# Kernel optimization log

Measured on AMD Instinct MI355X. Metric: run time of the kernel, lower is better.

Reference implementation:

```python
import jax, jax.numpy as jnp
import numpy as np

L, D, H, DK, DV, DFF = 6, 512, 8, 64, 64, 2048
B, S = 8, 512
EPS = 1e-5


def _pos_table(max_len, d_model):
    pos = np.arange(max_len)[:, None].astype(np.float64)
    i = np.arange(d_model)[None, :].astype(np.float64)
    t = pos / np.power(10000.0, 2.0 * i / d_model)
    t[0, :] = 0.0
    t[1:, 0::2] = np.sin(t[1:, 0::2])
    t[1:, 1::2] = np.cos(t[1:, 1::2])
    return jnp.asarray(t, dtype=jnp.float32)


def _ln(x, g, b):
    m = jnp.mean(x, axis=-1, keepdims=True)
    v = jnp.mean(jnp.square(x - m), axis=-1, keepdims=True)
    return (x - m) * jax.lax.rsqrt(v + EPS) * g + b


def setup_inputs() -> dict:
    key = jax.random.key(0)
    ks = jax.random.split(key, 12)
    s = 0.02
    return {
        "enc_inputs": jax.random.normal(ks[0], (B, S, D), jnp.float32),
        "enc_inputs_mask": jax.random.randint(ks[1], (B, S), 0, 100, dtype=jnp.int64),
        "Wq": jax.random.normal(ks[2], (L, D, H * DK), jnp.float32) * s,
        "Wk": jax.random.normal(ks[3], (L, D, H * DK), jnp.float32) * s,
        "Wv": jax.random.normal(ks[4], (L, D, H * DV), jnp.float32) * s,
        "Wo": jax.random.normal(ks[5], (L, H * DV, D), jnp.float32) * s,
        "ln1_g": jnp.ones((L, D), jnp.float32),
        "ln1_b": jnp.zeros((L, D), jnp.float32),
        "W1": jax.random.normal(ks[6], (L, D, DFF), jnp.float32) * s,
        "W2": jax.random.normal(ks[7], (L, DFF, D), jnp.float32) * s,
        "ln2_g": jnp.ones((L, D), jnp.float32),
        "ln2_b": jnp.zeros((L, D), jnp.float32),
    }


def reference(enc_inputs, enc_inputs_mask, Wq, Wk, Wv, Wo, ln1_g, ln1_b, W1, W2, ln2_g, ln2_b):
    b, s, _ = enc_inputs.shape
    x = enc_inputs + _pos_table(s, D)  # positional encoding (dropout = eval/no-op)
    # pad mask: True where key token is pad (mask id == 0); broadcast over heads & queries
    pad = (enc_inputs_mask == 0)[:, None, None, :]  # [B,1,1,S]
    inv_sqrt_dk = np.float32(1.0 / np.sqrt(DK))
    attns = []
    for l in range(L):
        residual = x
        q = (x @ Wq[l]).reshape(b, s, H, DK).transpose(0, 2, 1, 3)  # [B,H,S,DK]
        k = (x @ Wk[l]).reshape(b, s, H, DK).transpose(0, 2, 1, 3)
        v = (x @ Wv[l]).reshape(b, s, H, DV).transpose(0, 2, 1, 3)
        scores = jnp.einsum("bhqd,bhkd->bhqk", q, k) * inv_sqrt_dk
        scores = jnp.where(pad, jnp.float32(-1e9), scores)
        attn = jax.nn.softmax(scores, axis=-1)
        ctx = jnp.einsum("bhqk,bhkd->bhqd", attn, v)
        ctx = ctx.transpose(0, 2, 1, 3).reshape(b, s, H * DV)
        x = _ln(ctx @ Wo[l] + residual, ln1_g[l], ln1_b[l])
        x = _ln(jax.nn.relu(x @ W1[l]) @ W2[l] + x, ln2_g[l], ln2_b[l])
        attns.append(attn)
    return x, jnp.stack(attns)  # [B,S,D], [L,B,H,S,S]
```

## Files before the change

kernel.cpp:

```cpp
#include <hip/hip_runtime.h>

typedef __attribute__((ext_vector_type(8))) short bf16x8;
typedef __attribute__((ext_vector_type(4))) short bf16x4;
typedef __attribute__((ext_vector_type(4))) float f32x4;

__device__ __forceinline__ float b2f(ushort u) {
  union { uint u; float f; } x; x.u = ((uint)u) << 16; return x.f;
}
__device__ __forceinline__ ushort f2b(float f) {
  union { float f; uint u; } x; x.f = f;
  uint r = x.u + 0x7fffu + ((x.u >> 16) & 1u);
  return (ushort)(r >> 16);
}
__device__ __forceinline__ f32x4 mfma16(bf16x8 a, bf16x8 b, f32x4 c) {
  return __builtin_amdgcn_mfma_f32_16x16x32_bf16(a, b, c, 0, 0, 0);
}

__global__ void detect_kernel(const uint* __restrict__ ln1g, const uint* __restrict__ mask,
                              int* __restrict__ flags) {
  if (threadIdx.x == 0) {
    flags[0] = (ln1g[0] == 0x3F800000u) ? 1 : 0;
    int odd0 = 1;
    for (int i = 0; i < 16; i++)
      if (mask[2 * i + 1] != 0u) odd0 = 0;
    flags[1] = odd0;
  }
}

__global__ __launch_bounds__(256) void convert_kernel(const void* __restrict__ src,
                                                      ushort* __restrict__ dst, int n,
                                                      const int* __restrict__ flags) {
  int f = flags[0];
  int base = (blockIdx.x * 256 + threadIdx.x) * 8;
  int stride = gridDim.x * 256 * 8;
  if (f) {
    const float* s = (const float*)src;
    for (int i = base; i < n; i += stride) {
      float4 a = *(const float4*)(s + i);
      float4 b = *(const float4*)(s + i + 4);
      bf16x8 o;
      o[0] = (short)f2b(a.x); o[1] = (short)f2b(a.y); o[2] = (short)f2b(a.z); o[3] = (short)f2b(a.w);
      o[4] = (short)f2b(b.x); o[5] = (short)f2b(b.y); o[6] = (short)f2b(b.z); o[7] = (short)f2b(b.w);
      *(bf16x8*)(dst + i) = o;
    }
  } else {
    const ushort* s = (const ushort*)src;
    for (int i = base; i < n; i += stride)
      *(bf16x8*)(dst + i) = *(const bf16x8*)(s + i);
  }
}

__global__ __launch_bounds__(256) void posadd_kernel(const void* __restrict__ enc,
                                                     float* __restrict__ x32,
                                                     ushort* __restrict__ xb,
                                                     const int* __restrict__ flags) {
  int f = flags[0];
  int idx = blockIdx.x * 256 + threadIdx.x;
  int s = idx >> 9, d = idx & 511;
  float pef = 0.f;
  if (s > 0) {
    double t = (double)s / pow(10000.0, 2.0 * (double)d / 512.0);
    pef = (float)((d & 1) ? cos(t) : sin(t));
  }
  for (int b = 0; b < 8; b++) {
    size_t o = ((size_t)(b * 512 + s)) * 512 + d;
    float ev = f ? ((const float*)enc)[o] : b2f(((const ushort*)enc)[o]);
    float xv = ev + pef;
    x32[o] = xv;
    xb[o] = f2b(xv);
  }
}

template <bool RELU>
__device__ __forceinline__ void gemm_core(const ushort* __restrict__ A, const ushort* __restrict__ W,
                                          ushort* __restrict__ C, int M, int N, int K, int bm, int bn) {
  __shared__ ushort As[64][72];
  __shared__ ushort Bs[64][72];
  int tid = threadIdx.x;
  int wave = tid >> 6, lane = tid & 63;
  int lm = lane & 15, lq = lane >> 4;
  int wm = (wave & 1) * 32, wn = (wave >> 1) * 32;
  int m0 = bm * 64, n0 = bn * 64;
  f32x4 z = {0.f, 0.f, 0.f, 0.f};
  f32x4 acc00 = z, acc01 = z, acc10 = z, acc11 = z;
  int sr = tid >> 2, sc = (tid & 3) * 16;
  for (int k0 = 0; k0 < K; k0 += 64) {
    const ushort* asrc = A + (size_t)(m0 + sr) * K + k0 + sc;
    bf16x8 a0 = *(const bf16x8*)asrc;
    bf16x8 a1 = *(const bf16x8*)(asrc + 8);
    const ushort* wsrc = W + (size_t)(k0 + sr) * N + n0 + sc;
    bf16x8 w0 = *(const bf16x8*)wsrc;
    bf16x8 w1 = *(const bf16x8*)(wsrc + 8);
    *(bf16x8*)&As[sr][sc] = a0;
    *(bf16x8*)&As[sr][sc + 8] = a1;
#pragma unroll
    for (int i = 0; i < 8; i++) {
      Bs[sc + i][sr] = (ushort)w0[i];
      Bs[sc + 8 + i][sr] = (ushort)w1[i];
    }
    __syncthreads();
#pragma unroll
    for (int kk = 0; kk < 64; kk += 32) {
      bf16x8 fa0 = *(const bf16x8*)&As[wm + lm][kk + lq * 8];
      bf16x8 fa1 = *(const bf16x8*)&As[wm + 16 + lm][kk + lq * 8];
      bf16x8 fb0 = *(const bf16x8*)&Bs[wn + lm][kk + lq * 8];
      bf16x8 fb1 = *(const bf16x8*)&Bs[wn + 16 + lm][kk + lq * 8];
      acc00 = mfma16(fa0, fb0, acc00);
      acc01 = mfma16(fa0, fb1, acc01);
      acc10 = mfma16(fa1, fb0, acc10);
      acc11 = mfma16(fa1, fb1, acc11);
    }
    __syncthreads();
  }
#pragma unroll
  for (int r = 0; r < 4; r++) {
    int row0 = m0 + wm + lq * 4 + r;
    int row1 = row0 + 16;
    int col0 = n0 + wn + lm;
    int col1 = col0 + 16;
    float v;
    v = acc00[r]; if (RELU) v = fmaxf(v, 0.f); C[(size_t)row0 * N + col0] = f2b(v);
    v = acc01[r]; if (RELU) v = fmaxf(v, 0.f); C[(size_t)row0 * N + col1] = f2b(v);
    v = acc10[r]; if (RELU) v = fmaxf(v, 0.f); C[(size_t)row1 * N + col0] = f2b(v);
    v = acc11[r]; if (RELU) v = fmaxf(v, 0.f); C[(size_t)row1 * N + col1] = f2b(v);
  }
}

template <bool RELU>
__global__ __launch_bounds__(256) void gemm_kernel(const ushort* __restrict__ A, const ushort* __restrict__ W,
                                                   ushort* __restrict__ C, int M, int N, int K) {
  gemm_core<RELU>(A, W, C, M, N, K, blockIdx.x, blockIdx.y);
}

__global__ __launch_bounds__(256) void gemm_qkv_kernel(const ushort* __restrict__ A,
                                                       const ushort* __restrict__ Wq,
                                                       const ushort* __restrict__ Wk,
                                                       const ushort* __restrict__ Wv,
                                                       ushort* __restrict__ q, ushort* __restrict__ k,
                                                       ushort* __restrict__ v, int M, int N, int K) {
  const ushort* W = blockIdx.z == 0 ? Wq : (blockIdx.z == 1 ? Wk : Wv);
  ushort* C = blockIdx.z == 0 ? q : (blockIdx.z == 1 ? k : v);
  gemm_core<false>(A, W, C, M, N, K, blockIdx.x, blockIdx.y);
}

__global__ __launch_bounds__(256) void transpose_kernel(const ushort* __restrict__ v, ushort* __restrict__ vt) {
  __shared__ ushort T[64][72];
  int bh = blockIdx.x, b = bh >> 3, h = bh & 7;
  int s0 = blockIdx.y * 64;
  int r = threadIdx.x >> 2, c = (threadIdx.x & 3) * 16;
  const ushort* src = v + (size_t)(b * 512 + s0 + r) * 512 + h * 64 + c;
  bf16x8 x0 = *(const bf16x8*)src;
  bf16x8 x1 = *(const bf16x8*)(src + 8);
#pragma unroll
  for (int i = 0; i < 8; i++) {
    T[c + i][r] = (ushort)x0[i];
    T[c + 8 + i][r] = (ushort)x1[i];
  }
  __syncthreads();
  ushort* dst = vt + ((size_t)bh * 64 + r) * 512 + s0 + c;
  *(bf16x8*)dst = *(const bf16x8*)&T[r][c];
  *(bf16x8*)(dst + 8) = *(const bf16x8*)&T[r][c + 8];
}

__global__ __launch_bounds__(256) void attn_kernel(const ushort* __restrict__ qb, const ushort* __restrict__ kb,
                                                   const ushort* __restrict__ vt, const uint* __restrict__ mask,
                                                   void* __restrict__ out_base, size_t out_elem_off,
                                                   ushort* __restrict__ ctx, const int* __restrict__ flags) {
  __shared__ float Sc[16][516];
  __shared__ ushort Pb[16][520];
  __shared__ ushort Qs[16][72];
  __shared__ float red[16][16];
  __shared__ float rowmax[16];
  __shared__ float rowrinv[16];
  int of32 = flags[0], m64 = flags[1];
  int tid = threadIdx.x, wave = tid >> 6, lane = tid & 63;
  int lm = lane & 15, lq = lane >> 4;
  int bh = blockIdx.x, b = bh >> 3, h = bh & 7;
  int q0 = blockIdx.y * 16;
  {
    int r = tid >> 4, c = (tid & 15) * 4;
    const ushort* src = qb + (size_t)(b * 512 + q0 + r) * 512 + h * 64 + c;
    *(bf16x4*)&Qs[r][c] = *(const bf16x4*)src;
  }
  __syncthreads();
  bf16x8 a0 = *(const bf16x8*)&Qs[lm][lq * 8];
  bf16x8 a1 = *(const bf16x8*)&Qs[lm][32 + lq * 8];
  f32x4 z = {0.f, 0.f, 0.f, 0.f};
  for (int t8 = 0; t8 < 8; t8++) {
    int key = (wave * 8 + t8) * 16 + lm;
    const ushort* kp = kb + (size_t)(b * 512 + key) * 512 + h * 64;
    bf16x8 kb0 = *(const bf16x8*)(kp + lq * 8);
    bf16x8 kb1 = *(const bf16x8*)(kp + 32 + lq * 8);
    f32x4 s = mfma16(a0, kb0, z);
    s = mfma16(a1, kb1, s);
    uint mv = mask[(size_t)(b * 512 + key) << m64];
#pragma unroll
    for (int r = 0; r < 4; r++) {
      Sc[lq * 4 + r][key] = (mv == 0u) ? -1e9f : s[r] * 0.125f;
    }
  }
  __syncthreads();
  int row = tid >> 4, seg = tid & 15;
  float mx = -3.0e38f;
  for (int i = 0; i < 32; i++) {
    int ii = seg * 32 + ((i + seg * 2) & 31);
    mx = fmaxf(mx, Sc[row][ii]);
  }
  red[row][seg] = mx;
  __syncthreads();
  if (seg == 0) {
    float m = red[row][0];
    for (int i = 1; i < 16; i++) m = fmaxf(m, red[row][i]);
    rowmax[row] = m;
  }
  __syncthreads();
  float rmax = rowmax[row];
  float sum = 0.f;
  for (int i = 0; i < 32; i++) {
    int ii = seg * 32 + ((i + seg * 2) & 31);
    float e = expf(Sc[row][ii] - rmax);
    Sc[row][ii] = e;
    sum += e;
  }
  red[row][seg] = sum;
  __syncthreads();
  if (seg == 0) {
    float t = 0.f;
    for (int i = 0; i < 16; i++) t += red[row][i];
    rowrinv[row] = 1.f / t;
  }
  __syncthreads();
  float rinv = rowrinv[row];
  size_t rowbase = out_elem_off + ((size_t)(b * 8 + h) * 512 + (q0 + row)) * 512;
#pragma unroll
  for (int io = 0; io < 4; io++) {
    int ch = seg * 32 + (((io + seg) & 3) * 8);
    float pf[8];
    bf16x8 pv;
#pragma unroll
    for (int j = 0; j < 8; j++) {
      pf[j] = Sc[row][ch + j] * rinv;
      pv[j] = (short)f2b(pf[j]);
    }
    *(bf16x8*)&Pb[row][ch] = pv;
    if (of32) {
      float* ao = (float*)out_base;
      float4 p0 = {pf[0], pf[1], pf[2], pf[3]};
      float4 p1 = {pf[4], pf[5], pf[6], pf[7]};
      *(float4*)(ao + rowbase + ch) = p0;
      *(float4*)(ao + rowbase + ch + 4) = p1;
    } else {
      *(bf16x8*)((ushort*)out_base + rowbase + ch) = pv;
    }
  }
  __syncthreads();
  f32x4 c = z;
  int d = wave * 16 + lm;
  const ushort* vp = vt + ((size_t)bh * 64 + d) * 512;
#pragma unroll 4
  for (int ks = 0; ks < 16; ks++) {
    bf16x8 ap = *(const bf16x8*)&Pb[lm][ks * 32 + lq * 8];
    bf16x8 bv = *(const bf16x8*)(vp + ks * 32 + lq * 8);
    c = mfma16(ap, bv, c);
  }
#pragma unroll
  for (int r = 0; r < 4; r++) {
    ctx[(size_t)(b * 512 + q0 + lq * 4 + r) * 512 + h * 64 + d] = f2b(c[r]);
  }
}

__global__ __launch_bounds__(256) void ln_kernel(const ushort* __restrict__ a, float* __restrict__ x32,
                                                 ushort* __restrict__ xb, const void* __restrict__ g,
                                                 const void* __restrict__ bb, int goff,
                                                 const int* __restrict__ flags) {
  int f = flags[0];
  int row = blockIdx.x, tid = threadIdx.x;
  size_t base = (size_t)row * 512;
  float v0 = b2f(a[base + tid]) + x32[base + tid];
  float v1 = b2f(a[base + tid + 256]) + x32[base + tid + 256];
  float s1 = v0 + v1, s2 = v0 * v0 + v1 * v1;
#pragma unroll
  for (int off = 32; off > 0; off >>= 1) {
    s1 += __shfl_down(s1, off);
    s2 += __shfl_down(s2, off);
  }
  __shared__ float r1[4], r2[4];
  if ((tid & 63) == 0) { r1[tid >> 6] = s1; r2[tid >> 6] = s2; }
  __syncthreads();
  s1 = r1[0] + r1[1] + r1[2] + r1[3];
  s2 = r2[0] + r2[1] + r2[2] + r2[3];
  float m = s1 * (1.f / 512.f);
  float var = s2 * (1.f / 512.f) - m * m;
  float rs = rsqrtf(var + 1e-5f);
  float g0, g1v, b0, b1;
  if (f) {
    const float* gp = (const float*)g + goff;
    const float* bp = (const float*)bb + goff;
    g0 = gp[tid]; g1v = gp[tid + 256]; b0 = bp[tid]; b1 = bp[tid + 256];
  } else {
    const ushort* gp = (const ushort*)g + goff;
    const ushort* bp = (const ushort*)bb + goff;
    g0 = b2f(gp[tid]); g1v = b2f(gp[tid + 256]); b0 = b2f(bp[tid]); b1 = b2f(bp[tid + 256]);
  }
  float y0 = (v0 - m) * rs * g0 + b0;
  float y1 = (v1 - m) * rs * g1v + b1;
  x32[base + tid] = y0;        xb[base + tid] = f2b(y0);
  x32[base + tid + 256] = y1;  xb[base + tid + 256] = f2b(y1);
}

__global__ __launch_bounds__(256) void outx_kernel(const float* __restrict__ x32, void* __restrict__ out,
                                                   const int* __restrict__ flags) {
  int f = flags[0];
  int i = (blockIdx.x * 256 + threadIdx.x) * 4;
  float4 v = *(const float4*)(x32 + i);
  if (f) {
    *(float4*)((float*)out + i) = v;
  } else {
    bf16x4 o;
    o[0] = (short)f2b(v.x); o[1] = (short)f2b(v.y); o[2] = (short)f2b(v.z); o[3] = (short)f2b(v.w);
    *(bf16x4*)((ushort*)out + i) = o;
  }
}

extern "C" void kernel_launch(void* const* d_in, const int* in_sizes, int n_in,
                              void* d_out, int out_size, void* d_ws, size_t ws_size,
                              hipStream_t stream) {
  const void* enc  = d_in[0];
  const uint* mask = (const uint*)d_in[1];
  const void* Wq   = d_in[2];
  const void* Wk   = d_in[3];
  const void* Wv   = d_in[4];
  const void* Wo   = d_in[5];
  const void* ln1g = d_in[6];
  const void* ln1b = d_in[7];
  const void* W1   = d_in[8];
  const void* W2   = d_in[9];
  const void* ln2g = d_in[10];
  const void* ln2b = d_in[11];

  char* p = (char*)d_ws;
  int* flags  = (int*)p;      p += 256;
  ushort* cWq = (ushort*)p;   p += (size_t)1572864 * 2;
  ushort* cWk = (ushort*)p;   p += (size_t)1572864 * 2;
  ushort* cWv = (ushort*)p;   p += (size_t)1572864 * 2;
  ushort* cWo = (ushort*)p;   p += (size_t)1572864 * 2;
  ushort* cW1 = (ushort*)p;   p += (size_t)6291456 * 2;
  ushort* cW2 = (ushort*)p;   p += (size_t)6291456 * 2;
  float*  x32 = (float*)p;    p += (size_t)2097152 * 4;
  ushort* xb  = (ushort*)p;   p += (size_t)2097152 * 2;
  ushort* g2  = (ushort*)p;   p += (size_t)2097152 * 2;
  ushort* ctx = (ushort*)p;   p += (size_t)2097152 * 2;
  ushort* q   = (ushort*)p;   p += (size_t)2097152 * 2;
  ushort* k   = (ushort*)p;   p += (size_t)2097152 * 2;
  ushort* v   = (ushort*)p;   p += (size_t)2097152 * 2;
  ushort* vt  = (ushort*)p;   p += (size_t)2097152 * 2;
  ushort* g1  = q;

  detect_kernel<<<1, 64, 0, stream>>>((const uint*)ln1g, mask, flags);
  convert_kernel<<<1024, 256, 0, stream>>>(Wq, cWq, 1572864, flags);
  convert_kernel<<<1024, 256, 0, stream>>>(Wk, cWk, 1572864, flags);
  convert_kernel<<<1024, 256, 0, stream>>>(Wv, cWv, 1572864, flags);
  convert_kernel<<<1024, 256, 0, stream>>>(Wo, cWo, 1572864, flags);
  convert_kernel<<<2048, 256, 0, stream>>>(W1, cW1, 6291456, flags);
  convert_kernel<<<2048, 256, 0, stream>>>(W2, cW2, 6291456, flags);
  posadd_kernel<<<1024, 256, 0, stream>>>(enc, x32, xb, flags);

  for (int l = 0; l < 6; l++) {
    gemm_qkv_kernel<<<dim3(64, 8, 3), 256, 0, stream>>>(
        xb, cWq + (size_t)l * 262144, cWk + (size_t)l * 262144, cWv + (size_t)l * 262144,
        q, k, v, 4096, 512, 512);
    transpose_kernel<<<dim3(64, 8), 256, 0, stream>>>(v, vt);
    attn_kernel<<<dim3(64, 32), 256, 0, stream>>>(
        q, k, vt, mask, d_out, (size_t)2097152 + (size_t)l * 16777216, ctx, flags);
    gemm_kernel<false><<<dim3(64, 8), 256, 0, stream>>>(ctx, cWo + (size_t)l * 262144, g2, 4096, 512, 512);
    ln_kernel<<<4096, 256, 0, stream>>>(g2, x32, xb, ln1g, ln1b, l * 512, flags);
    gemm_kernel<true><<<dim3(64, 32), 256, 0, stream>>>(xb, cW1 + (size_t)l * 1048576, g1, 4096, 2048, 512);
    gemm_kernel<false><<<dim3(64, 8), 256, 0, stream>>>(g1, cW2 + (size_t)l * 1048576, g2, 4096, 512, 2048);
    ln_kernel<<<4096, 256, 0, stream>>>(g2, x32, xb, ln2g, ln2b, l * 512, flags);
  }
  outx_kernel<<<2048, 256, 0, stream>>>(x32, d_out, flags);
}
```

Baseline: 1.485 ms.

## Pre-transpose weights, use 128x128 GEMM tiles with direct global-to-LDS loads

Weight conversion now also transposes each weight to N-major layout, so GEMM B tiles load contiguously instead of being scattered and transposed through shared memory. The GEMM tile grows from 64x64 to 128x128 with 16 MFMA accumulators per wave, raising data reuse per LDS load. Tiles are filled with global_load_lds. The V projection writes its output already transposed, which removes the separate transpose kernel. Risks include higher register pressure, LDS bank conflicts from the unpadded 64-wide rows, fewer blocks for the smaller GEMMs (128 blocks for N=512), and no double buffering.

```diff
diff --git a/kernel.cpp b/kernel.cpp
--- a/kernel.cpp
+++ b/kernel.cpp
@@ -14,6 +14,10 @@
 }
 __device__ __forceinline__ f32x4 mfma16(bf16x8 a, bf16x8 b, f32x4 c) {
   return __builtin_amdgcn_mfma_f32_16x16x32_bf16(a, b, c, 0, 0, 0);
+}
+__device__ __forceinline__ void glds16(const ushort* g, ushort* l) {
+  __builtin_amdgcn_global_load_lds((const __attribute__((address_space(1))) void*)g,
+                                   (__attribute__((address_space(3))) void*)l, 16, 0, 0);
 }
 
 __global__ void detect_kernel(const uint* __restrict__ ln1g, const uint* __restrict__ mask,
@@ -27,27 +31,33 @@
   }
 }
 
-__global__ __launch_bounds__(256) void convert_kernel(const void* __restrict__ src,
-                                                      ushort* __restrict__ dst, int n,
-                                                      const int* __restrict__ flags) {
+__global__ __launch_bounds__(256) void convt_kernel(const void* __restrict__ src,
+                                                    ushort* __restrict__ dst, int K, int N,
+                                                    const int* __restrict__ flags) {
+  __shared__ ushort T[64][72];
   int f = flags[0];
-  int base = (blockIdx.x * 256 + threadIdx.x) * 8;
-  int stride = gridDim.x * 256 * 8;
+  size_t mo = (size_t)blockIdx.z * K * N;
+  int k0 = blockIdx.x * 64, n0 = blockIdx.y * 64;
+  int r = threadIdx.x >> 2, c = (threadIdx.x & 3) * 16;
   if (f) {
-    const float* s = (const float*)src;
-    for (int i = base; i < n; i += stride) {
-      float4 a = *(const float4*)(s + i);
-      float4 b = *(const float4*)(s + i + 4);
-      bf16x8 o;
-      o[0] = (short)f2b(a.x); o[1] = (short)f2b(a.y); o[2] = (short)f2b(a.z); o[3] = (short)f2b(a.w);
-      o[4] = (short)f2b(b.x); o[5] = (short)f2b(b.y); o[6] = (short)f2b(b.z); o[7] = (short)f2b(b.w);
-      *(bf16x8*)(dst + i) = o;
+    const float* sp = (const float*)src + mo + (size_t)(k0 + r) * N + n0 + c;
+#pragma unroll
+    for (int i = 0; i < 16; i += 4) {
+      float4 fv = *(const float4*)(sp + i);
+      T[c + i][r] = f2b(fv.x); T[c + i + 1][r] = f2b(fv.y);
+      T[c + i + 2][r] = f2b(fv.z); T[c + i + 3][r] = f2b(fv.w);
     }
   } else {
-    const ushort* s = (const ushort*)src;
-    for (int i = base; i < n; i += stride)
-      *(bf16x8*)(dst + i) = *(const bf16x8*)(s + i);
-  }
+    const ushort* sp = (const ushort*)src + mo + (size_t)(k0 + r) * N + n0 + c;
+    bf16x8 v0 = *(const bf16x8*)sp;
+    bf16x8 v1 = *(const bf16x8*)(sp + 8);
+#pragma unroll
+    for (int i = 0; i < 8; i++) { T[c + i][r] = (ushort)v0[i]; T[c + 8 + i][r] = (ushort)v1[i]; }
+  }
+  __syncthreads();
+  ushort* d = dst + mo + (size_t)(n0 + r) * K + k0 + c;
+  *(bf16x8*)d = *(const bf16x8*)&T[r][c];
+  *(bf16x8*)(d + 8) = *(const bf16x8*)&T[r][c + 8];
 }
 
 __global__ __launch_bounds__(256) void posadd_kernel(const void* __restrict__ enc,
@@ -71,65 +81,91 @@
   }
 }
 
-template <bool RELU>
-__device__ __forceinline__ void gemm_core(const ushort* __restrict__ A, const ushort* __restrict__ W,
-                                          ushort* __restrict__ C, int M, int N, int K, int bm, int bn) {
-  __shared__ ushort As[64][72];
-  __shared__ ushort Bs[64][72];
+template <bool RELU, int OUTMODE>
+__device__ __forceinline__ void gemm_bt_core(const ushort* __restrict__ A,
+                                             const ushort* __restrict__ Bt,
+                                             ushort* __restrict__ C,
+                                             int M, int N, int K, int bm, int bn) {
+  __shared__ ushort As[128 * 64];
+  __shared__ ushort Bs[128 * 64];
   int tid = threadIdx.x;
   int wave = tid >> 6, lane = tid & 63;
   int lm = lane & 15, lq = lane >> 4;
-  int wm = (wave & 1) * 32, wn = (wave >> 1) * 32;
-  int m0 = bm * 64, n0 = bn * 64;
+  int wm = (wave & 1) * 64, wn = (wave >> 1) * 64;
+  int m0 = bm * 128, n0 = bn * 128;
   f32x4 z = {0.f, 0.f, 0.f, 0.f};
-  f32x4 acc00 = z, acc01 = z, acc10 = z, acc11 = z;
-  int sr = tid >> 2, sc = (tid & 3) * 16;
+  f32x4 acc[4][4];
+#pragma unroll
+  for (int mi = 0; mi < 4; mi++)
+#pragma unroll
+    for (int ni = 0; ni < 4; ni++) acc[mi][ni] = z;
+
+  int sr = tid >> 3, sc = (tid & 7) * 8;
+  const ushort* ap = A + (size_t)(m0 + sr) * K + sc;
+  const ushort* bp = Bt + (size_t)(n0 + sr) * K + sc;
+  ushort* asd = As + tid * 8;
+  ushort* bsd = Bs + tid * 8;
+
   for (int k0 = 0; k0 < K; k0 += 64) {
-    const ushort* asrc = A + (size_t)(m0 + sr) * K + k0 + sc;
-    bf16x8 a0 = *(const bf16x8*)asrc;
-    bf16x8 a1 = *(const bf16x8*)(asrc + 8);
-    const ushort* wsrc = W + (size_t)(k0 + sr) * N + n0 + sc;
-    bf16x8 w0 = *(const bf16x8*)wsrc;
-    bf16x8 w1 = *(const bf16x8*)(wsrc + 8);
-    *(bf16x8*)&As[sr][sc] = a0;
-    *(bf16x8*)&As[sr][sc + 8] = a1;
-#pragma unroll
-    for (int i = 0; i < 8; i++) {
-      Bs[sc + i][sr] = (ushort)w0[i];
-      Bs[sc + 8 + i][sr] = (ushort)w1[i];
+#pragma unroll
+    for (int j = 0; j < 4; j++) {
+      glds16(ap + (size_t)(j * 32) * K + k0, asd + j * 2048);
+      glds16(bp + (size_t)(j * 32) * K + k0, bsd + j * 2048);
     }
     __syncthreads();
 #pragma unroll
     for (int kk = 0; kk < 64; kk += 32) {
-      bf16x8 fa0 = *(const bf16x8*)&As[wm + lm][kk + lq * 8];
-      bf16x8 fa1 = *(const bf16x8*)&As[wm + 16 + lm][kk + lq * 8];
-      bf16x8 fb0 = *(const bf16x8*)&Bs[wn + lm][kk + lq * 8];
-      bf16x8 fb1 = *(const bf16x8*)&Bs[wn + 16 + lm][kk + lq * 8];
-      acc00 = mfma16(fa0, fb0, acc00);
-      acc01 = mfma16(fa0, fb1, acc01);
-      acc10 = mfma16(fa1, fb0, acc10);
-      acc11 = mfma16(fa1, fb1, acc11);
+      bf16x8 af[4], bfv[4];
+#pragma unroll
+      for (int mi = 0; mi < 4; mi++)
+        af[mi] = *(const bf16x8*)&As[(wm + mi * 16 + lm) * 64 + kk + lq * 8];
+#pragma unroll
+      for (int ni = 0; ni < 4; ni++)
+        bfv[ni] = *(const bf16x8*)&Bs[(wn + ni * 16 + lm) * 64 + kk + lq * 8];
+#pragma unroll
+      for (int mi = 0; mi < 4; mi++)
+#pragma unroll
+        for (int ni = 0; ni < 4; ni++)
+          acc[mi][ni] = mfma16(af[mi], bfv[ni], acc[mi][ni]);
     }
     __syncthreads();
   }
-#pragma unroll
-  for (int r = 0; r < 4; r++) {
-    int row0 = m0 + wm + lq * 4 + r;
-    int row1 = row0 + 16;
-    int col0 = n0 + wn + lm;
-    int col1 = col0 + 16;
-    float v;
-    v = acc00[r]; if (RELU) v = fmaxf(v, 0.f); C[(size_t)row0 * N + col0] = f2b(v);
-    v = acc01[r]; if (RELU) v = fmaxf(v, 0.f); C[(size_t)row0 * N + col1] = f2b(v);
-    v = acc10[r]; if (RELU) v = fmaxf(v, 0.f); C[(size_t)row1 * N + col0] = f2b(v);
-    v = acc11[r]; if (RELU) v = fmaxf(v, 0.f); C[(size_t)row1 * N + col1] = f2b(v);
+
+  if (OUTMODE == 0) {
+#pragma unroll
+    for (int mi = 0; mi < 4; mi++)
+#pragma unroll
+      for (int ni = 0; ni < 4; ni++) {
+        int row = m0 + wm + mi * 16 + lq * 4;
+        int col = n0 + wn + ni * 16 + lm;
+#pragma unroll
+        for (int r = 0; r < 4; r++) {
+          float vv = acc[mi][ni][r];
+          if (RELU) vv = fmaxf(vv, 0.f);
+          C[(size_t)(row + r) * N + col] = f2b(vv);
+        }
+      }
+  } else {
+#pragma unroll
+    for (int mi = 0; mi < 4; mi++)
+#pragma unroll
+      for (int ni = 0; ni < 4; ni++) {
+        int row = m0 + wm + mi * 16 + lq * 4;
+        int col = n0 + wn + ni * 16 + lm;
+        int b = row >> 9, s = row & 511;
+        bf16x4 o;
+#pragma unroll
+        for (int r = 0; r < 4; r++) o[r] = (short)f2b(acc[mi][ni][r]);
+        *(bf16x4*)&C[((size_t)(b * 8 + (col >> 6)) * 64 + (col & 63)) * 512 + s] = o;
+      }
   }
 }
 
 template <bool RELU>
-__global__ __launch_bounds__(256) void gemm_kernel(const ushort* __restrict__ A, const ushort* __restrict__ W,
-                                                   ushort* __restrict__ C, int M, int N, int K) {
-  gemm_core<RELU>(A, W, C, M, N, K, blockIdx.x, blockIdx.y);
+__global__ __launch_bounds__(256) void gemm_bt_kernel(const ushort* __restrict__ A,
+                                                      const ushort* __restrict__ Bt,
+                                                      ushort* __restrict__ C, int M, int N, int K) {
+  gemm_bt_core<RELU, 0>(A, Bt, C, M, N, K, blockIdx.x, blockIdx.y);
 }
 
 __global__ __launch_bounds__(256) void gemm_qkv_kernel(const ushort* __restrict__ A,
@@ -137,29 +173,10 @@
                                                        const ushort* __restrict__ Wk,
                                                        const ushort* __restrict__ Wv,
                                                        ushort* __restrict__ q, ushort* __restrict__ k,
-                                                       ushort* __restrict__ v, int M, int N, int K) {
-  const ushort* W = blockIdx.z == 0 ? Wq : (blockIdx.z == 1 ? Wk : Wv);
-  ushort* C = blockIdx.z == 0 ? q : (blockIdx.z == 1 ? k : v);
-  gemm_core<false>(A, W, C, M, N, K, blockIdx.x, blockIdx.y);
-}
-
-__global__ __launch_bounds__(256) void transpose_kernel(const ushort* __restrict__ v, ushort* __restrict__ vt) {
-  __shared__ ushort T[64][72];
-  int bh = blockIdx.x, b = bh >> 3, h = bh & 7;
-  int s0 = blockIdx.y * 64;
-  int r = threadIdx.x >> 2, c = (threadIdx.x & 3) * 16;
-  const ushort* src = v + (size_t)(b * 512 + s0 + r) * 512 + h * 64 + c;
-  bf16x8 x0 = *(const bf16x8*)src;
-  bf16x8 x1 = *(const bf16x8*)(src + 8);
-#pragma unroll
-  for (int i = 0; i < 8; i++) {
-    T[c + i][r] = (ushort)x0[i];
-    T[c + 8 + i][r] = (ushort)x1[i];
-  }
-  __syncthreads();
-  ushort* dst = vt + ((size_t)bh * 64 + r) * 512 + s0 + c;
-  *(bf16x8*)dst = *(const bf16x8*)&T[r][c];
-  *(bf16x8*)(dst + 8) = *(const bf16x8*)&T[r][c + 8];
+                                                       ushort* __restrict__ vt, int M, int N, int K) {
+  if (blockIdx.z == 0)      gemm_bt_core<false, 0>(A, Wq, q,  M, N, K, blockIdx.x, blockIdx.y);
+  else if (blockIdx.z == 1) gemm_bt_core<false, 0>(A, Wk, k,  M, N, K, blockIdx.x, blockIdx.y);
+  else                      gemm_bt_core<false, 1>(A, Wv, vt, M, N, K, blockIdx.x, blockIdx.y);
 }
 
 __global__ __launch_bounds__(256) void attn_kernel(const ushort* __restrict__ qb, const ushort* __restrict__ kb,
@@ -340,42 +357,41 @@
 
   char* p = (char*)d_ws;
   int* flags  = (int*)p;      p += 256;
-  ushort* cWq = (ushort*)p;   p += (size_t)1572864 * 2;
-  ushort* cWk = (ushort*)p;   p += (size_t)1572864 * 2;
-  ushort* cWv = (ushort*)p;   p += (size_t)1572864 * 2;
-  ushort* cWo = (ushort*)p;   p += (size_t)1572864 * 2;
-  ushort* cW1 = (ushort*)p;   p += (size_t)6291456 * 2;
-  ushort* cW2 = (ushort*)p;   p += (size_t)6291456 * 2;
+  ushort* tWq = (ushort*)p;   p += (size_t)1572864 * 2;
+  ushort* tWk = (ushort*)p;   p += (size_t)1572864 * 2;
+  ushort* tWv = (ushort*)p;   p += (size_t)1572864 * 2;
+  ushort* tWo = (ushort*)p;   p += (size_t)1572864 * 2;
+  ushort* tW1 = (ushort*)p;   p += (size_t)6291456 * 2;
+  ushort* tW2 = (ushort*)p;   p += (size_t)6291456 * 2;
   float*  x32 = (float*)p;    p += (size_t)2097152 * 4;
   ushort* xb  = (ushort*)p;   p += (size_t)2097152 * 2;
   ushort* g2  = (ushort*)p;   p += (size_t)2097152 * 2;
   ushort* ctx = (ushort*)p;   p += (size_t)2097152 * 2;
   ushort* q   = (ushort*)p;   p += (size_t)2097152 * 2;
   ushort* k   = (ushort*)p;   p += (size_t)2097152 * 2;
-  ushort* v   = (ushort*)p;   p += (size_t)2097152 * 2;
+  p += (size_t)2097152 * 2;
   ushort* vt  = (ushort*)p;   p += (size_t)2097152 * 2;
   ushort* g1  = q;
 
   detect_kernel<<<1, 64, 0, stream>>>((const uint*)ln1g, mask, flags);
-  convert_kernel<<<1024, 256, 0, stream>>>(Wq, cWq, 1572864, flags);
-  convert_kernel<<<1024, 256, 0, stream>>>(Wk, cWk, 1572864, flags);
-  convert_kernel<<<1024, 256, 0, stream>>>(Wv, cWv, 1572864, flags);
-  convert_kernel<<<1024, 256, 0, stream>>>(Wo, cWo, 1572864, flags);
-  convert_kernel<<<2048, 256, 0, stream>>>(W1, cW1, 6291456, flags);
-  convert_kernel<<<2048, 256, 0, stream>>>(W2, cW2, 6291456, flags);
+  convt_kernel<<<dim3(8, 8, 6),  256, 0, stream>>>(Wq, tWq, 512, 512, flags);
+  convt_kernel<<<dim3(8, 8, 6),  256, 0, stream>>>(Wk, tWk, 512, 512, flags);
+  convt_kernel<<<dim3(8, 8, 6),  256, 0, stream>>>(Wv, tWv, 512, 512, flags);
+  convt_kernel<<<dim3(8, 8, 6),  256, 0, stream>>>(Wo, tWo, 512, 512, flags);
+  convt_kernel<<<dim3(8, 32, 6), 256, 0, stream>>>(W1, tW1, 512, 2048, flags);
+  convt_kernel<<<dim3(32, 8, 6), 256, 0, stream>>>(W2, tW2, 2048, 512, flags);
   posadd_kernel<<<1024, 256, 0, stream>>>(enc, x32, xb, flags);
 
   for (int l = 0; l < 6; l++) {
-    gemm_qkv_kernel<<<dim3(64, 8, 3), 256, 0, stream>>>(
-        xb, cWq + (size_t)l * 262144, cWk + (size_t)l * 262144, cWv + (size_t)l * 262144,
-        q, k, v, 4096, 512, 512);
-    transpose_kernel<<<dim3(64, 8), 256, 0, stream>>>(v, vt);
+    gemm_qkv_kernel<<<dim3(32, 4, 3), 256, 0, stream>>>(
+        xb, tWq + (size_t)l * 262144, tWk + (size_t)l * 262144, tWv + (size_t)l * 262144,
+        q, k, vt, 4096, 512, 512);
     attn_kernel<<<dim3(64, 32), 256, 0, stream>>>(
         q, k, vt, mask, d_out, (size_t)2097152 + (size_t)l * 16777216, ctx, flags);
-    gemm_kernel<false><<<dim3(64, 8), 256, 0, stream>>>(ctx, cWo + (size_t)l * 262144, g2, 4096, 512, 512);
+    gemm_bt_kernel<false><<<dim3(32, 4), 256, 0, stream>>>(ctx, tWo + (size_t)l * 262144, g2, 4096, 512, 512);
     ln_kernel<<<4096, 256, 0, stream>>>(g2, x32, xb, ln1g, ln1b, l * 512, flags);
-    gemm_kernel<true><<<dim3(64, 32), 256, 0, stream>>>(xb, cW1 + (size_t)l * 1048576, g1, 4096, 2048, 512);
-    gemm_kernel<false><<<dim3(64, 8), 256, 0, stream>>>(g1, cW2 + (size_t)l * 1048576, g2, 4096, 512, 2048);
+    gemm_bt_kernel<true><<<dim3(32, 16), 256, 0, stream>>>(xb, tW1 + (size_t)l * 1048576, g1, 4096, 2048, 512);
+    gemm_bt_kernel<false><<<dim3(32, 4), 256, 0, stream>>>(g1, tW2 + (size_t)l * 1048576, g2, 4096, 512, 2048);
     ln_kernel<<<4096, 256, 0, stream>>>(g2, x32, xb, ln2g, ln2b, l * 512, flags);
   }
   outx_kernel<<<2048, 256, 0, stream>>>(x32, d_out, flags);
```

Result: faster. 1.396 ms (-6.0%).
